# Kernel optimization log

Hardware: AMD Instinct MI355X
Metric: run time of the kernel (lower is better)

Reference implementation:

```python
import jax, jax.numpy as jnp
import numpy as np

B, N, D_IN, D_OUT, E = 16, 16384, 128, 128, 65536
LN_EPS = 1e-5


def setup_inputs() -> dict:
    key = jax.random.key(0)
    k1, k2, k3, k4 = jax.random.split(key, 4)
    x = jax.random.normal(k1, (B, N, D_IN), dtype=jnp.float32)
    edge_index = jax.random.randint(k2, (2, E), 0, N, dtype=jnp.int64)
    W_self = jax.random.normal(k3, (D_OUT, D_IN), dtype=jnp.float32) / np.sqrt(D_IN)
    W_neigh = jax.random.normal(k4, (D_OUT, D_IN), dtype=jnp.float32) / np.sqrt(D_IN)
    return {
        "x": x,
        "edge_index": edge_index,
        "batch_size": B,
        "W_self": W_self,
        "W_neigh": W_neigh,
        "bias": jnp.zeros((D_OUT,), jnp.float32),
        "gamma": jnp.ones((D_OUT,), jnp.float32),
        "beta": jnp.zeros((D_OUT,), jnp.float32),
    }


def reference(x, edge_index, batch_size, W_self, W_neigh, bias, gamma, beta):
    b, n, d = x.shape
    src, dst = edge_index[0], edge_index[1]
    # expand edge index for disjoint batched graphs: add per-graph node offsets
    offsets = (jnp.arange(batch_size, dtype=src.dtype) * n)[:, None]  # [B,1]
    src_e = (src[None, :] + offsets).reshape(-1)  # [B*E]
    dst_e = (dst[None, :] + offsets).reshape(-1)
    x_flat = x.reshape(batch_size * n, d)
    # scatter-sum neighbor features and degrees, then mean
    agg = jax.ops.segment_sum(x_flat[src_e], dst_e, num_segments=batch_size * n)
    deg = jax.ops.segment_sum(jnp.ones_like(dst_e, dtype=x_flat.dtype), dst_e,
                              num_segments=batch_size * n)
    neigh = agg / jnp.maximum(deg, 1.0)[:, None]
    out = x_flat @ W_self.T + neigh @ W_neigh.T + bias  # [B*N, D_OUT]
    # LayerNorm over last dim
    mu = jnp.mean(out, axis=-1, keepdims=True)
    var = jnp.mean(jnp.square(out - mu), axis=-1, keepdims=True)
    out = (out - mu) * jax.lax.rsqrt(var + LN_EPS) * gamma + beta
    out = jax.nn.relu(out)
    return out.reshape(batch_size, n, -1)
```

## Files before the change

kernel.cpp:

```cpp
#include <hip/hip_runtime.h>
#include <hip/hip_bf16.h>
#include <stdint.h>

#define B_ 16
#define N_ 16384
#define D_ 128
#define E_ 65536

typedef __attribute__((ext_vector_type(8))) __bf16 bf16x8;
typedef __attribute__((ext_vector_type(4))) float f32x4;

__device__ __forceinline__ uint16_t f2bf(float f) {
    union { float f; uint32_t u; } v;
    v.f = f;
    uint32_t u = v.u;
    uint32_t r = (u + 0x7fffu + ((u >> 16) & 1u)) >> 16;
    return (uint16_t)r;
}

__device__ __forceinline__ bool ei_is64(const int* __restrict__ ei, int t) {
    int w = ei[2 * (t & 63) + 1];
    return __ballot(w != 0) == 0ull;
}

__global__ void k_cntpack(const int* __restrict__ ei,
                          const float* __restrict__ wself,
                          const float* __restrict__ wneigh,
                          int* __restrict__ deg,
                          uint16_t* __restrict__ wpack) {
    int t = threadIdx.x;
    int bid = blockIdx.x;
    if (bid < 256) {
        bool is64 = ei_is64(ei, t);
        int e = bid * 256 + t;
        int d = is64 ? ei[2 * (E_ + e)] : ei[E_ + e];
        atomicAdd(&deg[d], 1);
    } else {
        int g = (bid - 256) * 256 + t;
        int j = g & 7;
        int lane = (g >> 3) & 63;
        int nt = (g >> 9) & 7;
        int ks = g >> 12;
        int k = ks * 32 + (lane >> 4) * 8 + j;
        int n = nt * 16 + (lane & 15);
        float v = (k < 128) ? wself[n * 128 + k] : wneigh[n * 128 + (k - 128)];
        wpack[g] = f2bf(v);
    }
}

__global__ void k_scan(const int* __restrict__ deg, int* __restrict__ off,
                       int* __restrict__ cur) {
    __shared__ int ps[256];
    int t = threadIdx.x;
    int vals[64];
    const int4* dv = (const int4*)(deg + t * 64);
    int s = 0;
#pragma unroll
    for (int i = 0; i < 16; i++) {
        int4 v = dv[i];
        vals[4 * i + 0] = v.x; vals[4 * i + 1] = v.y;
        vals[4 * i + 2] = v.z; vals[4 * i + 3] = v.w;
        s += v.x + v.y + v.z + v.w;
    }
    ps[t] = s;
    __syncthreads();
#pragma unroll
    for (int st = 1; st < 256; st <<= 1) {
        int add = (t >= st) ? ps[t - st] : 0;
        __syncthreads();
        ps[t] += add;
        __syncthreads();
    }
    int run = ps[t] - s;
#pragma unroll
    for (int i = 0; i < 64; i++) {
        off[t * 64 + i] = run;
        cur[t * 64 + i] = run;
        run += vals[i];
    }
    if (t == 255) off[N_] = run;
}

__global__ void k_fill(const int* __restrict__ ei, int* __restrict__ cur,
                       int* __restrict__ adj) {
    int t = threadIdx.x;
    bool is64 = ei_is64(ei, t);
    int e = blockIdx.x * 256 + t;
    int s = is64 ? ei[2 * e] : ei[e];
    int d = is64 ? ei[2 * (E_ + e)] : ei[E_ + e];
    int p = atomicAdd(&cur[d], 1);
    adj[p] = s;
}

__global__ __launch_bounds__(256) void k_agg(const float* __restrict__ x,
                                             const int* __restrict__ off,
                                             const int* __restrict__ adj,
                                             unsigned char* __restrict__ scratch) {
    int t = threadIdx.x;
    int g = blockIdx.x & 15;
    int chunk = blockIdx.x >> 4;
    int hw = t >> 5, l = t & 31;
    int node = chunk * 8 + hw;
    int o0 = off[node], o1 = off[node + 1];
    const float* xg = x + (size_t)g * N_ * D_;
    float ax = 0.f, ay = 0.f, az = 0.f, aw = 0.f;
    int e = o0;
    for (; e + 1 < o1; e += 2) {
        int s0 = adj[e], s1 = adj[e + 1];
        float4 v0 = *(const float4*)(xg + (size_t)s0 * D_ + l * 4);
        float4 v1 = *(const float4*)(xg + (size_t)s1 * D_ + l * 4);
        ax += v0.x + v1.x; ay += v0.y + v1.y;
        az += v0.z + v1.z; aw += v0.w + v1.w;
    }
    if (e < o1) {
        int s0 = adj[e];
        float4 v0 = *(const float4*)(xg + (size_t)s0 * D_ + l * 4);
        ax += v0.x; ay += v0.y; az += v0.z; aw += v0.w;
    }
    float sc = 1.f / fmaxf((float)(o1 - o0), 1.f);
    uint32_t p0 = (uint32_t)f2bf(ax * sc) | ((uint32_t)f2bf(ay * sc) << 16);
    uint32_t p1 = (uint32_t)f2bf(az * sc) | ((uint32_t)f2bf(aw * sc) << 16);
    uint2 pv; pv.x = p0; pv.y = p1;
    *(uint2*)(scratch + ((size_t)g * N_ + node) * 512 + 256 + l * 8) = pv;
}

__global__ __launch_bounds__(256) void k_main(
    const float* __restrict__ x,
    const uint16_t* __restrict__ wpack,
    const float* __restrict__ bias,
    const float* __restrict__ gamma_,
    const float* __restrict__ beta_,
    float* out) {
    __shared__ __align__(16) unsigned char smem[33792];
    __shared__ float prm[3][128];
    uint16_t* As = (uint16_t*)smem;
    float* Cs = (float*)smem;

    int t = threadIdx.x;
    int b = blockIdx.x & 15;
    int tile = blockIdx.x >> 4;
    int node0 = tile * 64;

    if (t < 128) {
        prm[0][t] = bias[t];
        prm[1][t] = gamma_[t];
        prm[2][t] = beta_[t];
    }

    int r = t >> 2;
    int q = t & 3;
    int node = node0 + r;
    const size_t xrow_base = ((size_t)b * N_ + node) * D_;
    int mt = r >> 4, m = r & 15;

    {
        const float4* xv = (const float4*)(x + xrow_base);
#pragma unroll
        for (int c = 0; c < 4; c++) {
            float4 a0 = xv[q * 8 + 2 * c + 0];
            float4 a1 = xv[q * 8 + 2 * c + 1];
            float f[8] = {a0.x, a0.y, a0.z, a0.w, a1.x, a1.y, a1.z, a1.w};
            uint32_t pk[4];
#pragma unroll
            for (int p = 0; p < 4; p++)
                pk[p] = (uint32_t)f2bf(f[2 * p]) | ((uint32_t)f2bf(f[2 * p + 1]) << 16);
            int kc = q * 4 + c;
            int ks = kc >> 2, qd = kc & 3;
            uint4 v = make_uint4(pk[0], pk[1], pk[2], pk[3]);
            *(uint4*)&As[(((ks * 4 + mt) * 64) + qd * 16 + m) * 8] = v;
        }
    }

    {
        const uint4* nv = (const uint4*)((const unsigned char*)out +
                                         ((size_t)b * N_ + node) * 512 + 256);
#pragma unroll
        for (int c = 0; c < 4; c++) {
            uint4 v = nv[q * 4 + c];
            int kc = 16 + q * 4 + c;
            int ks = kc >> 2, qd = kc & 3;
            *(uint4*)&As[(((ks * 4 + mt) * 64) + qd * 16 + m) * 8] = v;
        }
    }

    __syncthreads();

    int wv = t >> 6;
    int lane = t & 63;
    f32x4 accv[4][2];
#pragma unroll
    for (int i = 0; i < 4; i++)
#pragma unroll
        for (int j = 0; j < 2; j++) {
            f32x4 z = {0.f, 0.f, 0.f, 0.f};
            accv[i][j] = z;
        }

    const uint4* wp = (const uint4*)wpack;
#pragma unroll
    for (int ks = 0; ks < 8; ks++) {
        uint4 b0u = wp[(ks * 8 + 2 * wv + 0) * 64 + lane];
        uint4 b1u = wp[(ks * 8 + 2 * wv + 1) * 64 + lane];
        bf16x8 bf0 = __builtin_bit_cast(bf16x8, b0u);
        bf16x8 bf1 = __builtin_bit_cast(bf16x8, b1u);
#pragma unroll
        for (int mtt = 0; mtt < 4; mtt++) {
            bf16x8 a = *(const bf16x8*)&As[((ks * 4 + mtt) * 64 + lane) * 8];
            accv[mtt][0] = __builtin_amdgcn_mfma_f32_16x16x32_bf16(a, bf0, accv[mtt][0], 0, 0, 0);
            accv[mtt][1] = __builtin_amdgcn_mfma_f32_16x16x32_bf16(a, bf1, accv[mtt][1], 0, 0, 0);
        }
    }

    __syncthreads();

#pragma unroll
    for (int mtt = 0; mtt < 4; mtt++)
#pragma unroll
        for (int ntl = 0; ntl < 2; ntl++)
#pragma unroll
            for (int rg = 0; rg < 4; rg++) {
                int row = mtt * 16 + (lane >> 4) * 4 + rg;
                int col = (2 * wv + ntl) * 16 + (lane & 15);
                Cs[row * 132 + (col >> 5) * 33 + (col & 31)] = accv[mtt][ntl][rg];
            }

    __syncthreads();

    {
        float s1 = 0.f, s2 = 0.f;
#pragma unroll
        for (int i = 0; i < 32; i++) {
            float v = Cs[r * 132 + q * 33 + i] + prm[0][q * 32 + i];
            s1 += v;
            s2 += v * v;
        }
        s1 += __shfl_xor(s1, 1, 64);
        s2 += __shfl_xor(s2, 1, 64);
        s1 += __shfl_xor(s1, 2, 64);
        s2 += __shfl_xor(s2, 2, 64);
        float mu = s1 * (1.f / 128.f);
        float var = s2 * (1.f / 128.f) - mu * mu;
        float rstd = rsqrtf(var + 1e-5f);

        float* orow = out + xrow_base;
#pragma unroll
        for (int c = 0; c < 8; c++) {
            float4 o;
            float tmp[4];
#pragma unroll
            for (int j = 0; j < 4; j++) {
                int i0 = c * 4 + j;
                int d0 = q * 32 + i0;
                float v = Cs[r * 132 + q * 33 + i0] + prm[0][d0];
                tmp[j] = fmaxf((v - mu) * rstd * prm[1][d0] + prm[2][d0], 0.f);
            }
            o.x = tmp[0]; o.y = tmp[1]; o.z = tmp[2]; o.w = tmp[3];
            *(float4*)&orow[q * 32 + c * 4] = o;
        }
    }
}

extern "C" void kernel_launch(void* const* d_in, const int* in_sizes, int n_in,
                              void* d_out, int out_size, void* d_ws, size_t ws_size,
                              hipStream_t stream) {
    (void)in_sizes; (void)n_in; (void)out_size; (void)ws_size;
    const float* x      = (const float*)d_in[0];
    const int*   ei     = (const int*)d_in[1];
    const float* wself  = (const float*)d_in[3];
    const float* wneigh = (const float*)d_in[4];
    const float* bias   = (const float*)d_in[5];
    const float* gma    = (const float*)d_in[6];
    const float* bta    = (const float*)d_in[7];
    float* out = (float*)d_out;

    char* ws = (char*)d_ws;
    int* deg        = (int*)(ws);
    int* off        = (int*)(ws + 65536);
    int* cur        = (int*)(ws + 131584);
    int* adj        = (int*)(ws + 197120);
    uint16_t* wpack = (uint16_t*)(ws + 459264);

    hipMemsetAsync(deg, 0, N_ * sizeof(int), stream);
    k_cntpack<<<384, 256, 0, stream>>>(ei, wself, wneigh, deg, wpack);
    k_scan<<<1, 256, 0, stream>>>(deg, off, cur);
    k_fill<<<E_ / 256, 256, 0, stream>>>(ei, cur, adj);
    k_agg<<<B_ * N_ / 8, 256, 0, stream>>>(x, off, adj, (unsigned char*)out);
    k_main<<<B_ * (N_ / 64), 256, 0, stream>>>(x, wpack, bias, gma, bta, out);
}
```

Before: 388.7 us.

## Fuse all stages into one cooperative persistent kernel with bf16 x staging

Replaces the memset and five separate kernels with a single cooperative kernel that uses grid-wide syncs between phases: degree count, weight pack, scan, CSR fill, x-to-bf16 conversion, neighbor aggregation and the MFMA GEMM+LayerNorm. It adds a pass that converts all of x to bf16 into the output buffer, so the gather reads half the bytes and the GEMM reads bf16 directly. The aim is to cut launch gaps and gather bandwidth. The cost is an extra full read/write pass over x, six grid barriers, a single-block scan that leaves most of the grid idle, and persistent-loop occupancy limits.

```diff
diff --git a/kernel.cpp b/kernel.cpp
--- a/kernel.cpp
+++ b/kernel.cpp
@@ -1,11 +1,15 @@
 #include <hip/hip_runtime.h>
+#include <hip/hip_cooperative_groups.h>
 #include <hip/hip_bf16.h>
 #include <stdint.h>
+
+namespace cg = cooperative_groups;
 
 #define B_ 16
 #define N_ 16384
 #define D_ 128
 #define E_ 65536
+#define NTILES (B_ * (N_ / 64))
 
 typedef __attribute__((ext_vector_type(8))) __bf16 bf16x8;
 typedef __attribute__((ext_vector_type(4))) float f32x4;
@@ -14,219 +18,210 @@
     union { float f; uint32_t u; } v;
     v.f = f;
     uint32_t u = v.u;
-    uint32_t r = (u + 0x7fffu + ((u >> 16) & 1u)) >> 16;
-    return (uint16_t)r;
-}
-
-__device__ __forceinline__ bool ei_is64(const int* __restrict__ ei, int t) {
-    int w = ei[2 * (t & 63) + 1];
-    return __ballot(w != 0) == 0ull;
-}
-
-__global__ void k_cntpack(const int* __restrict__ ei,
-                          const float* __restrict__ wself,
-                          const float* __restrict__ wneigh,
-                          int* __restrict__ deg,
-                          uint16_t* __restrict__ wpack) {
+    return (uint16_t)((u + 0x7fffu + ((u >> 16) & 1u)) >> 16);
+}
+__device__ __forceinline__ float bf2f(uint32_t b) {
+    union { uint32_t u; float f; } v;
+    v.u = b << 16;
+    return v.f;
+}
+
+__global__ __launch_bounds__(256, 4) void k_all(
+    const float* __restrict__ x, const int* __restrict__ ei,
+    const float* __restrict__ wself, const float* __restrict__ wneigh,
+    const float* __restrict__ bias, const float* __restrict__ gamma_,
+    const float* __restrict__ beta_, float* out,
+    int* deg, int* off, int* cur, int* adj, uint16_t* wpack) {
+    cg::grid_group gg = cg::this_grid();
+    __shared__ __align__(16) unsigned char smem[33792];
+    __shared__ float prm[3][128];
+
     int t = threadIdx.x;
     int bid = blockIdx.x;
-    if (bid < 256) {
-        bool is64 = ei_is64(ei, t);
-        int e = bid * 256 + t;
+    int nth = gridDim.x * 256;
+    int tg = bid * 256 + t;
+    unsigned char* scratch = (unsigned char*)out;
+
+    bool is64;
+    {
+        int w = ei[2 * (t & 63) + 1];
+        is64 = (__ballot(w != 0) == 0ull);
+    }
+
+    for (int i = tg; i < N_; i += nth) deg[i] = 0;
+    __threadfence();
+    gg.sync();
+
+    for (int e = tg; e < E_; e += nth) {
         int d = is64 ? ei[2 * (E_ + e)] : ei[E_ + e];
         atomicAdd(&deg[d], 1);
-    } else {
-        int g = (bid - 256) * 256 + t;
+    }
+    for (int g = tg; g < 32768; g += nth) {
         int j = g & 7;
         int lane = (g >> 3) & 63;
-        int nt = (g >> 9) & 7;
+        int nt2 = (g >> 9) & 7;
         int ks = g >> 12;
         int k = ks * 32 + (lane >> 4) * 8 + j;
-        int n = nt * 16 + (lane & 15);
+        int n = nt2 * 16 + (lane & 15);
         float v = (k < 128) ? wself[n * 128 + k] : wneigh[n * 128 + (k - 128)];
         wpack[g] = f2bf(v);
     }
-}
-
-__global__ void k_scan(const int* __restrict__ deg, int* __restrict__ off,
-                       int* __restrict__ cur) {
-    __shared__ int ps[256];
-    int t = threadIdx.x;
-    int vals[64];
-    const int4* dv = (const int4*)(deg + t * 64);
-    int s = 0;
-#pragma unroll
-    for (int i = 0; i < 16; i++) {
-        int4 v = dv[i];
-        vals[4 * i + 0] = v.x; vals[4 * i + 1] = v.y;
-        vals[4 * i + 2] = v.z; vals[4 * i + 3] = v.w;
-        s += v.x + v.y + v.z + v.w;
-    }
-    ps[t] = s;
-    __syncthreads();
-#pragma unroll
-    for (int st = 1; st < 256; st <<= 1) {
-        int add = (t >= st) ? ps[t - st] : 0;
-        __syncthreads();
-        ps[t] += add;
-        __syncthreads();
-    }
-    int run = ps[t] - s;
-#pragma unroll
-    for (int i = 0; i < 64; i++) {
-        off[t * 64 + i] = run;
-        cur[t * 64 + i] = run;
-        run += vals[i];
-    }
-    if (t == 255) off[N_] = run;
-}
-
-__global__ void k_fill(const int* __restrict__ ei, int* __restrict__ cur,
-                       int* __restrict__ adj) {
-    int t = threadIdx.x;
-    bool is64 = ei_is64(ei, t);
-    int e = blockIdx.x * 256 + t;
-    int s = is64 ? ei[2 * e] : ei[e];
-    int d = is64 ? ei[2 * (E_ + e)] : ei[E_ + e];
-    int p = atomicAdd(&cur[d], 1);
-    adj[p] = s;
-}
-
-__global__ __launch_bounds__(256) void k_agg(const float* __restrict__ x,
-                                             const int* __restrict__ off,
-                                             const int* __restrict__ adj,
-                                             unsigned char* __restrict__ scratch) {
-    int t = threadIdx.x;
-    int g = blockIdx.x & 15;
-    int chunk = blockIdx.x >> 4;
-    int hw = t >> 5, l = t & 31;
-    int node = chunk * 8 + hw;
-    int o0 = off[node], o1 = off[node + 1];
-    const float* xg = x + (size_t)g * N_ * D_;
-    float ax = 0.f, ay = 0.f, az = 0.f, aw = 0.f;
-    int e = o0;
-    for (; e + 1 < o1; e += 2) {
-        int s0 = adj[e], s1 = adj[e + 1];
-        float4 v0 = *(const float4*)(xg + (size_t)s0 * D_ + l * 4);
-        float4 v1 = *(const float4*)(xg + (size_t)s1 * D_ + l * 4);
-        ax += v0.x + v1.x; ay += v0.y + v1.y;
-        az += v0.z + v1.z; aw += v0.w + v1.w;
-    }
-    if (e < o1) {
-        int s0 = adj[e];
-        float4 v0 = *(const float4*)(xg + (size_t)s0 * D_ + l * 4);
-        ax += v0.x; ay += v0.y; az += v0.z; aw += v0.w;
-    }
-    float sc = 1.f / fmaxf((float)(o1 - o0), 1.f);
-    uint32_t p0 = (uint32_t)f2bf(ax * sc) | ((uint32_t)f2bf(ay * sc) << 16);
-    uint32_t p1 = (uint32_t)f2bf(az * sc) | ((uint32_t)f2bf(aw * sc) << 16);
-    uint2 pv; pv.x = p0; pv.y = p1;
-    *(uint2*)(scratch + ((size_t)g * N_ + node) * 512 + 256 + l * 8) = pv;
-}
-
-__global__ __launch_bounds__(256) void k_main(
-    const float* __restrict__ x,
-    const uint16_t* __restrict__ wpack,
-    const float* __restrict__ bias,
-    const float* __restrict__ gamma_,
-    const float* __restrict__ beta_,
-    float* out) {
-    __shared__ __align__(16) unsigned char smem[33792];
-    __shared__ float prm[3][128];
-    uint16_t* As = (uint16_t*)smem;
-    float* Cs = (float*)smem;
-
-    int t = threadIdx.x;
-    int b = blockIdx.x & 15;
-    int tile = blockIdx.x >> 4;
-    int node0 = tile * 64;
+    __threadfence();
+    gg.sync();
+
+    if (bid == 0) {
+        int* ps = (int*)smem;
+        int base = t * 64;
+        int s = 0;
+        for (int i = 0; i < 64; i += 4) {
+            int4 v = *(const int4*)(deg + base + i);
+            s += v.x + v.y + v.z + v.w;
+        }
+        ps[t] = s;
+        __syncthreads();
+        for (int st = 1; st < 256; st <<= 1) {
+            int add = (t >= st) ? ps[t - st] : 0;
+            __syncthreads();
+            ps[t] += add;
+            __syncthreads();
+        }
+        int run = ps[t] - s;
+        for (int i = 0; i < 64; i += 4) {
+            int4 v = *(const int4*)(deg + base + i);
+            off[base + i] = run; cur[base + i] = run; run += v.x;
+            off[base + i + 1] = run; cur[base + i + 1] = run; run += v.y;
+            off[base + i + 2] = run; cur[base + i + 2] = run; run += v.z;
+            off[base + i + 3] = run; cur[base + i + 3] = run; run += v.w;
+        }
+        if (t == 255) off[N_] = run;
+    }
+    __threadfence();
+    gg.sync();
+
+    for (int e = tg; e < E_; e += nth) {
+        int s = is64 ? ei[2 * e] : ei[e];
+        int d = is64 ? ei[2 * (E_ + e)] : ei[E_ + e];
+        int p = atomicAdd(&cur[d], 1);
+        adj[p] = s;
+    }
+    __threadfence();
+    gg.sync();
+
+    for (int gi = tg; gi < B_ * N_ * D_ / 4; gi += nth) {
+        float4 v = ((const float4*)x)[gi];
+        int row = gi >> 5, c4 = gi & 31;
+        uint2 pv;
+        pv.x = (uint32_t)f2bf(v.x) | ((uint32_t)f2bf(v.y) << 16);
+        pv.y = (uint32_t)f2bf(v.z) | ((uint32_t)f2bf(v.w) << 16);
+        *(uint2*)(scratch + (size_t)row * 512 + c4 * 8) = pv;
+    }
+    __threadfence();
+    gg.sync();
+
+    {
+        int l = t & 31;
+        int hw = tg >> 5;
+        int nhw = nth >> 5;
+        for (int nid = hw; nid < B_ * N_; nid += nhw) {
+            int g = nid & 15, node = nid >> 4;
+            int o0 = off[node], o1 = off[node + 1];
+            const unsigned char* xg = scratch + (size_t)g * N_ * 512;
+            float a0 = 0.f, a1 = 0.f, a2 = 0.f, a3 = 0.f;
+            int e = o0;
+            for (; e + 1 < o1; e += 2) {
+                int s0 = adj[e], s1 = adj[e + 1];
+                uint2 v0 = *(const uint2*)(xg + (size_t)s0 * 512 + l * 8);
+                uint2 v1 = *(const uint2*)(xg + (size_t)s1 * 512 + l * 8);
+                a0 += bf2f(v0.x & 0xffffu) + bf2f(v1.x & 0xffffu);
+                a1 += bf2f(v0.x >> 16) + bf2f(v1.x >> 16);
+                a2 += bf2f(v0.y & 0xffffu) + bf2f(v1.y & 0xffffu);
+                a3 += bf2f(v0.y >> 16) + bf2f(v1.y >> 16);
+            }
+            if (e < o1) {
+                int s0 = adj[e];
+                uint2 v0 = *(const uint2*)(xg + (size_t)s0 * 512 + l * 8);
+                a0 += bf2f(v0.x & 0xffffu);
+                a1 += bf2f(v0.x >> 16);
+                a2 += bf2f(v0.y & 0xffffu);
+                a3 += bf2f(v0.y >> 16);
+            }
+            float sc = 1.f / fmaxf((float)(o1 - o0), 1.f);
+            uint2 pv;
+            pv.x = (uint32_t)f2bf(a0 * sc) | ((uint32_t)f2bf(a1 * sc) << 16);
+            pv.y = (uint32_t)f2bf(a2 * sc) | ((uint32_t)f2bf(a3 * sc) << 16);
+            *(uint2*)(scratch + ((size_t)g * N_ + node) * 512 + 256 + l * 8) = pv;
+        }
+    }
+    __threadfence();
+    gg.sync();
 
     if (t < 128) {
         prm[0][t] = bias[t];
         prm[1][t] = gamma_[t];
         prm[2][t] = beta_[t];
     }
-
+    uint16_t* As = (uint16_t*)smem;
+    float* Cs = (float*)smem;
     int r = t >> 2;
     int q = t & 3;
-    int node = node0 + r;
-    const size_t xrow_base = ((size_t)b * N_ + node) * D_;
+    int wv = t >> 6, lane = t & 63;
     int mt = r >> 4, m = r & 15;
 
-    {
-        const float4* xv = (const float4*)(x + xrow_base);
+    for (int tid = bid; tid < NTILES; tid += gridDim.x) {
+        int b = tid & 15, tile = tid >> 4;
+        size_t row = (size_t)b * N_ + tile * 64 + r;
+
+        const uint4* sv = (const uint4*)(scratch + row * 512);
 #pragma unroll
         for (int c = 0; c < 4; c++) {
-            float4 a0 = xv[q * 8 + 2 * c + 0];
-            float4 a1 = xv[q * 8 + 2 * c + 1];
-            float f[8] = {a0.x, a0.y, a0.z, a0.w, a1.x, a1.y, a1.z, a1.w};
-            uint32_t pk[4];
-#pragma unroll
-            for (int p = 0; p < 4; p++)
-                pk[p] = (uint32_t)f2bf(f[2 * p]) | ((uint32_t)f2bf(f[2 * p + 1]) << 16);
-            int kc = q * 4 + c;
-            int ks = kc >> 2, qd = kc & 3;
-            uint4 v = make_uint4(pk[0], pk[1], pk[2], pk[3]);
+            uint4 v = sv[q * 4 + c];
+            int kc = q * 4 + c, ks = kc >> 2, qd = kc & 3;
             *(uint4*)&As[(((ks * 4 + mt) * 64) + qd * 16 + m) * 8] = v;
         }
-    }
-
-    {
-        const uint4* nv = (const uint4*)((const unsigned char*)out +
-                                         ((size_t)b * N_ + node) * 512 + 256);
 #pragma unroll
         for (int c = 0; c < 4; c++) {
-            uint4 v = nv[q * 4 + c];
-            int kc = 16 + q * 4 + c;
-            int ks = kc >> 2, qd = kc & 3;
+            uint4 v = sv[16 + q * 4 + c];
+            int kc = 16 + q * 4 + c, ks = kc >> 2, qd = kc & 3;
             *(uint4*)&As[(((ks * 4 + mt) * 64) + qd * 16 + m) * 8] = v;
         }
-    }
-
-    __syncthreads();
-
-    int wv = t >> 6;
-    int lane = t & 63;
-    f32x4 accv[4][2];
-#pragma unroll
-    for (int i = 0; i < 4; i++)
-#pragma unroll
-        for (int j = 0; j < 2; j++) {
-            f32x4 z = {0.f, 0.f, 0.f, 0.f};
-            accv[i][j] = z;
-        }
-
-    const uint4* wp = (const uint4*)wpack;
-#pragma unroll
-    for (int ks = 0; ks < 8; ks++) {
-        uint4 b0u = wp[(ks * 8 + 2 * wv + 0) * 64 + lane];
-        uint4 b1u = wp[(ks * 8 + 2 * wv + 1) * 64 + lane];
-        bf16x8 bf0 = __builtin_bit_cast(bf16x8, b0u);
-        bf16x8 bf1 = __builtin_bit_cast(bf16x8, b1u);
-#pragma unroll
-        for (int mtt = 0; mtt < 4; mtt++) {
-            bf16x8 a = *(const bf16x8*)&As[((ks * 4 + mtt) * 64 + lane) * 8];
-            accv[mtt][0] = __builtin_amdgcn_mfma_f32_16x16x32_bf16(a, bf0, accv[mtt][0], 0, 0, 0);
-            accv[mtt][1] = __builtin_amdgcn_mfma_f32_16x16x32_bf16(a, bf1, accv[mtt][1], 0, 0, 0);
-        }
-    }
-
-    __syncthreads();
-
-#pragma unroll
-    for (int mtt = 0; mtt < 4; mtt++)
-#pragma unroll
-        for (int ntl = 0; ntl < 2; ntl++)
-#pragma unroll
-            for (int rg = 0; rg < 4; rg++) {
-                int row = mtt * 16 + (lane >> 4) * 4 + rg;
-                int col = (2 * wv + ntl) * 16 + (lane & 15);
-                Cs[row * 132 + (col >> 5) * 33 + (col & 31)] = accv[mtt][ntl][rg];
-            }
-
-    __syncthreads();
-
-    {
+        __syncthreads();
+
+        f32x4 accv[4][2];
+#pragma unroll
+        for (int i = 0; i < 4; i++)
+#pragma unroll
+            for (int j = 0; j < 2; j++) {
+                f32x4 z = {0.f, 0.f, 0.f, 0.f};
+                accv[i][j] = z;
+            }
+        const uint4* wp = (const uint4*)wpack;
+#pragma unroll
+        for (int ks = 0; ks < 8; ks++) {
+            uint4 b0u = wp[(ks * 8 + 2 * wv + 0) * 64 + lane];
+            uint4 b1u = wp[(ks * 8 + 2 * wv + 1) * 64 + lane];
+            bf16x8 bf0 = __builtin_bit_cast(bf16x8, b0u);
+            bf16x8 bf1 = __builtin_bit_cast(bf16x8, b1u);
+#pragma unroll
+            for (int mtt = 0; mtt < 4; mtt++) {
+                bf16x8 a = *(const bf16x8*)&As[((ks * 4 + mtt) * 64 + lane) * 8];
+                accv[mtt][0] = __builtin_amdgcn_mfma_f32_16x16x32_bf16(a, bf0, accv[mtt][0], 0, 0, 0);
+                accv[mtt][1] = __builtin_amdgcn_mfma_f32_16x16x32_bf16(a, bf1, accv[mtt][1], 0, 0, 0);
+            }
+        }
+        __syncthreads();
+
+#pragma unroll
+        for (int mtt = 0; mtt < 4; mtt++)
+#pragma unroll
+            for (int ntl = 0; ntl < 2; ntl++)
+#pragma unroll
+                for (int rg = 0; rg < 4; rg++) {
+                    int rr = mtt * 16 + (lane >> 4) * 4 + rg;
+                    int cc = (2 * wv + ntl) * 16 + (lane & 15);
+                    Cs[rr * 132 + (cc >> 5) * 33 + (cc & 31)] = accv[mtt][ntl][rg];
+                }
+        __syncthreads();
+
         float s1 = 0.f, s2 = 0.f;
 #pragma unroll
         for (int i = 0; i < 32; i++) {
@@ -242,10 +237,9 @@
         float var = s2 * (1.f / 128.f) - mu * mu;
         float rstd = rsqrtf(var + 1e-5f);
 
-        float* orow = out + xrow_base;
+        float* orow = out + row * (size_t)D_;
 #pragma unroll
         for (int c = 0; c < 8; c++) {
-            float4 o;
             float tmp[4];
 #pragma unroll
             for (int j = 0; j < 4; j++) {
@@ -254,9 +248,11 @@
                 float v = Cs[r * 132 + q * 33 + i0] + prm[0][d0];
                 tmp[j] = fmaxf((v - mu) * rstd * prm[1][d0] + prm[2][d0], 0.f);
             }
+            float4 o;
             o.x = tmp[0]; o.y = tmp[1]; o.z = tmp[2]; o.w = tmp[3];
             *(float4*)&orow[q * 32 + c * 4] = o;
         }
+        __syncthreads();
     }
 }
 
@@ -280,10 +276,16 @@
     int* adj        = (int*)(ws + 197120);
     uint16_t* wpack = (uint16_t*)(ws + 459264);
 
-    hipMemsetAsync(deg, 0, N_ * sizeof(int), stream);
-    k_cntpack<<<384, 256, 0, stream>>>(ei, wself, wneigh, deg, wpack);
-    k_scan<<<1, 256, 0, stream>>>(deg, off, cur);
-    k_fill<<<E_ / 256, 256, 0, stream>>>(ei, cur, adj);
-    k_agg<<<B_ * N_ / 8, 256, 0, stream>>>(x, off, adj, (unsigned char*)out);
-    k_main<<<B_ * (N_ / 64), 256, 0, stream>>>(x, wpack, bias, gma, bta, out);
-}
+    int maxB = 0;
+    if (hipOccupancyMaxActiveBlocksPerMultiprocessor(&maxB, k_all, 256, 0) != hipSuccess ||
+        maxB < 1)
+        maxB = 2;
+    int grid = 256 * maxB;
+    if (grid > 1024) grid = 1024;
+
+    void* args[] = {(void*)&x,   (void*)&ei,  (void*)&wself, (void*)&wneigh,
+                    (void*)&bias, (void*)&gma, (void*)&bta,   (void*)&out,
+                    (void*)&deg,  (void*)&off, (void*)&cur,   (void*)&adj,
+                    (void*)&wpack};
+    hipLaunchCooperativeKernel((const void*)k_all, dim3(grid), dim3(256), args, 0, stream);
+}
```

New measurement: 1.085 ms. +179.0%, slower.
